# Performance work log

Hardware: AMD Instinct MI355X
Metric: run time of the kernel (lower is better)

Reference implementation:

```python
import jax, jax.numpy as jnp
import numpy as np
from jax import lax

EPSILON = 1e-12


def _sobel_kernels(n1=1, n2=2, n3=2):
    Sx = np.asarray([[[-n1, 0, n1], [-n2, 0, n2], [-n1, 0, n1]],
                     [[-n2, 0, n2], [-n3 * n2, 0, n3 * n2], [-n2, 0, n2]],
                     [[-n1, 0, n1], [-n2, 0, n2], [-n1, 0, n1]]])
    Sy = np.asarray([[[-n1, -n2, -n1], [0, 0, 0], [n1, n2, n1]],
                     [[-n2, -n3 * n2, -n2], [0, 0, 0], [n2, n3 * n2, n2]],
                     [[-n1, -n2, -n1], [0, 0, 0], [n1, n2, n1]]])
    Sz = np.asarray([[[-n1, -n2, -n1], [-n2, -n3 * n2, -n2], [-n1, -n2, -n1]],
                     [[0, 0, 0], [0, 0, 0], [0, 0, 0]],
                     [[n1, n2, n1], [n2, n3 * n2, n2], [n1, n2, n1]]])
    Sd11 = np.asarray([[[0, n1, n2], [-n1, 0, n1], [-n2, -n1, 0]],
                       [[0, n2, n2 * n3], [-n2, 0, n2], [-n2 * n3, -n2, 0]],
                       [[0, n1, n2], [-n1, 0, n1], [-n2, -n1, 0]]])
    Sd12 = np.asarray([[[-n2, -n1, 0], [-n1, 0, n1], [0, n1, n2]],
                       [[-n2 * n3, -n2, 0], [-n2, 0, n2], [0, n2, n2 * n3]],
                       [[-n2, -n1, 0], [-n1, 0, n1], [0, n1, n2]]])
    Sd21 = Sd11.T
    Sd22 = Sd12.T
    Sd31 = np.asarray([-S.T for S in Sd11.T])
    Sd32 = np.asarray([S.T for S in Sd12.T])
    ks = np.stack([Sx, Sy, Sz, Sd11, Sd12, Sd21, Sd22, Sd31, Sd32]).astype(np.float32)
    return jnp.asarray(ks[:, None])  # [9, 1, 3, 3, 3] (OIDHW)


_KERNELS = _sobel_kernels(1, 2, 2)


def _edge_magnitude(img):
    # img: [B, C, H, W, D]. Per-channel convs are summed over C in the original;
    # by linearity of conv, sum channels first, then run all 9 stencils at once.
    C = img.shape[1]
    x = jnp.sum(img, axis=1, keepdims=True)  # [B, 1, H, W, D]
    g = lax.conv_general_dilated(
        x, _KERNELS, window_strides=(1, 1, 1), padding='SAME',
        dimension_numbers=('NCDHW', 'OIDHW', 'NCDHW'))  # [B, 9, H, W, D]
    mag = jnp.sqrt(jnp.sum(g * g, axis=1, keepdims=True) + EPSILON)
    return mag / C  # (1/C) * sqrt(sum_sq + eps), matches operator precedence


def setup_inputs() -> dict:
    key = jax.random.key(0)
    k1, k2 = jax.random.split(key)
    shape = (2, 2, 128, 128, 128)
    y = jax.random.normal(k1, shape, dtype=jnp.float32)
    yp = jax.random.normal(k2, shape, dtype=jnp.float32)
    return {"y": y, "yp": yp}


def reference(y, yp):
    y_edge = _edge_magnitude(y)
    yp_edge = _edge_magnitude(yp)
    return jnp.mean((y_edge - yp_edge) ** 2)  # nn.MSELoss default 'mean'
```

## Files before the change

### kernel.cpp

```cpp
#include <hip/hip_runtime.h>


namespace {

constexpr int YX = 128 * 128;
constexpr ptrdiff_t CS = (ptrdiff_t)128 * YX;
constexpr int ZC = 16;
constexpr float INV_N = 1.0f / 4194304.0f;

__device__ __forceinline__ float edge_mag_half(const float* __restrict__ Ca,
                                               const float* __restrict__ Cb,
                                               const float* __restrict__ Cc) {
  const float g1  = __builtin_fmaf(2.0f, Cb[0], Ca[0] + Cc[0]);
  const float g2  = __builtin_fmaf(2.0f, Cb[1], Ca[1] + Cc[1]);
  const float g3  = Cc[2] - Ca[2];
  const float Azx = __builtin_fmaf(2.0f, Cb[3], Ca[3] + Cc[3]);
  const float Azy = __builtin_fmaf(2.0f, Cb[4], Ca[4] + Cc[4]);
  const float Axz = Cc[5] - Ca[5];
  const float Axy = g2 - Cb[1];
  const float Ayx = g1 - Cb[0];
  const float Ayz = Cc[6] - Ca[6];
  const float g4 = Azx - Azy, g5 = Azx + Azy;
  const float g6 = Axz - Axy, g7 = Axz + Axy;
  const float g8 = Ayx - Ayz, g9 = Ayx + Ayz;
  float s = __builtin_fmaf(g1, g1, 1e-12f);
  s = __builtin_fmaf(g2, g2, s); s = __builtin_fmaf(g3, g3, s);
  s = __builtin_fmaf(g4, g4, s); s = __builtin_fmaf(g5, g5, s);
  s = __builtin_fmaf(g6, g6, s); s = __builtin_fmaf(g7, g7, s);
  s = __builtin_fmaf(g8, g8, s); s = __builtin_fmaf(g9, g9, s);
  return 0.5f * sqrtf(s);
}

__device__ __forceinline__ void combos7(const float* __restrict__ s,
                                        const float* __restrict__ h,
                                        bool l0, bool l63, int seg,
                                        float* __restrict__ C) {
  const float t  = s[0] + s[2];
  const float ys = __builtin_fmaf(2.0f, s[1], t);
  const float ye = t + s[1];
  const float yd = s[2] - s[0];
  const float th  = h[0] + h[2];
  const float hys = __builtin_fmaf(2.0f, h[1], th);
  const float hye = th + h[1];
  const float hyd = h[2] - h[0];
  float ysL = __shfl_up(ys, 1),  ydL = __shfl_up(yd, 1),  yeL = __shfl_up(ye, 1);
  float ysR = __shfl_down(ys, 1), ydR = __shfl_down(yd, 1), yeR = __shfl_down(ye, 1);
  const float eLs = seg ? hys : 0.0f, eLd = seg ? hyd : 0.0f, eLe = seg ? hye : 0.0f;
  const float eRs = seg ? 0.0f : hys, eRd = seg ? 0.0f : hyd, eRe = seg ? 0.0f : hye;
  ysL = l0 ? eLs : ysL;  ydL = l0 ? eLd : ydL;  yeL = l0 ? eLe : yeL;
  ysR = l63 ? eRs : ysR; ydR = l63 ? eRd : ydR; yeR = l63 ? eRe : yeR;
  C[0] = ysR - ysL;
  const float tds = ydL + ydR;
  C[1] = __builtin_fmaf(2.0f, yd, tds);
  C[4] = tds + yd;
  const float tss = ysL + ysR;
  C[2] = __builtin_fmaf(2.0f, ys, tss);
  C[6] = tss + ys;
  C[3] = yeR - yeL;
  const float tes = yeL + yeR;
  C[5] = __builtin_fmaf(2.0f, ye, tes);
}

__global__ __launch_bounds__(256)
void gme_loss_kernel(const float* __restrict__ y,
                     const float* __restrict__ yp,
                     float* __restrict__ out) {
  const int tid  = threadIdx.x;
  const int lane = tid & 63;
  const int wv   = tid >> 6;
  const int yy   = blockIdx.x * 4 + wv;
  const int seg  = blockIdx.y >> 3;
  const int z0   = (blockIdx.y & 7) * ZC;
  const int b    = blockIdx.z;
  const int px   = seg * 64 + lane;
  const bool l0 = (lane == 0), l63 = (lane == 63);
  const bool isEdge = seg ? l0 : l63;
  const ptrdiff_t hd = seg ? -1 : 1;
  const float w0 = (yy > 0)   ? 1.0f : 0.0f;
  const float w2 = (yy < 127) ? 1.0f : 0.0f;
  const int r0 = (yy > 0) ? yy - 1 : 0;
  const int r2 = (yy < 127) ? yy + 1 : 127;

  const float* Yb = y  + (ptrdiff_t)b * 2 * CS;
  const float* Pb = yp + (ptrdiff_t)b * 2 * CS;
  const ptrdiff_t o0 = (ptrdiff_t)r0 * 128 + px;
  const ptrdiff_t o1 = (ptrdiff_t)yy * 128 + px;
  const ptrdiff_t o2 = (ptrdiff_t)r2 * 128 + px;

  float arA[12], arB[12], hr[12];
#pragma unroll
  for (int j = 0; j < 12; ++j) { arA[j] = 0.f; arB[j] = 0.f; hr[j] = 0.f; }

  auto issue_ar = [&](int zl, float* __restrict__ a) {
    if ((unsigned)zl < 128u) {
      const float* Yz = Yb + (ptrdiff_t)zl * YX;
      const float* Pz = Pb + (ptrdiff_t)zl * YX;
      a[0]  = Yz[o0]; a[1]  = Yz[o0 + CS];
      a[2]  = Yz[o1]; a[3]  = Yz[o1 + CS];
      a[4]  = Yz[o2]; a[5]  = Yz[o2 + CS];
      a[6]  = Pz[o0]; a[7]  = Pz[o0 + CS];
      a[8]  = Pz[o1]; a[9]  = Pz[o1 + CS];
      a[10] = Pz[o2]; a[11] = Pz[o2 + CS];
    } else {
#pragma unroll
      for (int j = 0; j < 12; ++j) a[j] = 0.0f;
    }
  };
  auto issue_hr = [&](int zl) {
    if ((unsigned)zl < 128u) {
      if (isEdge) {
        const float* Yz = Yb + (ptrdiff_t)zl * YX;
        const float* Pz = Pb + (ptrdiff_t)zl * YX;
        hr[0]  = Yz[o0 + hd]; hr[1]  = Yz[o0 + CS + hd];
        hr[2]  = Yz[o1 + hd]; hr[3]  = Yz[o1 + CS + hd];
        hr[4]  = Yz[o2 + hd]; hr[5]  = Yz[o2 + CS + hd];
        hr[6]  = Pz[o0 + hd]; hr[7]  = Pz[o0 + CS + hd];
        hr[8]  = Pz[o1 + hd]; hr[9]  = Pz[o1 + CS + hd];
        hr[10] = Pz[o2 + hd]; hr[11] = Pz[o2 + CS + hd];
      }
    } else {
#pragma unroll
      for (int j = 0; j < 12; ++j) hr[j] = 0.0f;
    }
  };

  float sY[3], hY[3], sP[3], hP[3];
  auto consume = [&](const float* __restrict__ a) {
    sY[0] = (a[0] + a[1])  * w0;  sY[1] = a[2] + a[3];  sY[2] = (a[4] + a[5])  * w2;
    sP[0] = (a[6] + a[7])  * w0;  sP[1] = a[8] + a[9];  sP[2] = (a[10] + a[11]) * w2;
    hY[0] = (hr[0] + hr[1]) * w0; hY[1] = hr[2] + hr[3]; hY[2] = (hr[4] + hr[5]) * w2;
    hP[0] = (hr[6] + hr[7]) * w0; hP[1] = hr[8] + hr[9]; hP[2] = (hr[10] + hr[11]) * w2;
  };

  float KY[3][7], KP[3][7];
  float acc = 0.0f;

  issue_ar(z0 - 1, arA);
  issue_hr(z0 - 1);
  issue_ar(z0, arB);

#pragma unroll 6
  for (int i = 0; i < ZC + 2; ++i) {
    const int zc = z0 - 1 + i;
    consume((i & 1) ? arB : arA);
    const int zl_hr = (i <= ZC)     ? (zc + 1) : 128;
    const int zl_ar = (i <= ZC - 1) ? (zc + 2) : 128;
    issue_hr(zl_hr);
    issue_ar(zl_ar, (i & 1) ? arB : arA);
    combos7(sY, hY, l0, l63, seg, KY[i % 3]);
    combos7(sP, hP, l0, l63, seg, KP[i % 3]);
    if (i >= 2) {
      const float my = edge_mag_half(KY[(i + 1) % 3], KY[(i + 2) % 3], KY[i % 3]);
      const float mp = edge_mag_half(KP[(i + 1) % 3], KP[(i + 2) % 3], KP[i % 3]);
      const float d = my - mp;
      acc = __builtin_fmaf(d, d, acc);
    }
  }

#pragma unroll
  for (int off = 32; off > 0; off >>= 1) acc += __shfl_down(acc, off);
  __shared__ float red[4];
  if (lane == 0) red[wv] = acc;
  __syncthreads();
  if (tid == 0) atomicAdd(out, (red[0] + red[1] + red[2] + red[3]) * INV_N);
}

}

extern "C" void kernel_launch(void* const* d_in, const int* in_sizes, int n_in,
                              void* d_out, int out_size, void* d_ws, size_t ws_size,
                              hipStream_t stream) {
  const float* y  = (const float*)d_in[0];
  const float* yp = (const float*)d_in[1];
  float* out = (float*)d_out;

  hipMemsetAsync(out, 0, sizeof(float), stream);

  dim3 block(256, 1, 1);
  dim3 grid(32,
            16,
            2);
  gme_loss_kernel<<<grid, block, 0, stream>>>(y, yp, out);
}
```

Baseline: 123.4 us.

## Process two x-columns per lane to drop halo loads and vectorize

Each lane now owns two adjacent x positions, so one wavefront covers a full 128-wide row. This removes the split into two x-segments and the extra edge-lane halo loads, and turns the loads into 8-byte float2 accesses. The z-chunk per block is halved to keep the same grid size, the z loop is fully unrolled, and launch bounds request 3 blocks per CU. Register pressure roughly doubles because every value is now a pair, which could cut occupancy. The shorter z chunk also raises the fraction of redundant z-halo reads per block.

After: 171.7 us. 39.2% more time.

```diff
diff --git a/kernel.cpp b/kernel.cpp
--- a/kernel.cpp
+++ b/kernel.cpp
@@ -5,63 +5,71 @@
 
 constexpr int YX = 128 * 128;
 constexpr ptrdiff_t CS = (ptrdiff_t)128 * YX;
-constexpr int ZC = 16;
+constexpr int ZC = 8;
 constexpr float INV_N = 1.0f / 4194304.0f;
 
-__device__ __forceinline__ float edge_mag_half(const float* __restrict__ Ca,
-                                               const float* __restrict__ Cb,
-                                               const float* __restrict__ Cc) {
-  const float g1  = __builtin_fmaf(2.0f, Cb[0], Ca[0] + Cc[0]);
-  const float g2  = __builtin_fmaf(2.0f, Cb[1], Ca[1] + Cc[1]);
-  const float g3  = Cc[2] - Ca[2];
-  const float Azx = __builtin_fmaf(2.0f, Cb[3], Ca[3] + Cc[3]);
-  const float Azy = __builtin_fmaf(2.0f, Cb[4], Ca[4] + Cc[4]);
-  const float Axz = Cc[5] - Ca[5];
-  const float Axy = g2 - Cb[1];
-  const float Ayx = g1 - Cb[0];
-  const float Ayz = Cc[6] - Ca[6];
-  const float g4 = Azx - Azy, g5 = Azx + Azy;
-  const float g6 = Axz - Axy, g7 = Axz + Axy;
-  const float g8 = Ayx - Ayz, g9 = Ayx + Ayz;
-  float s = __builtin_fmaf(g1, g1, 1e-12f);
-  s = __builtin_fmaf(g2, g2, s); s = __builtin_fmaf(g3, g3, s);
-  s = __builtin_fmaf(g4, g4, s); s = __builtin_fmaf(g5, g5, s);
-  s = __builtin_fmaf(g6, g6, s); s = __builtin_fmaf(g7, g7, s);
-  s = __builtin_fmaf(g8, g8, s); s = __builtin_fmaf(g9, g9, s);
-  return 0.5f * sqrtf(s);
+struct V2 { float x, y; };
+__device__ __forceinline__ V2 v2(float a, float b) { V2 r; r.x = a; r.y = b; return r; }
+__device__ __forceinline__ V2 operator+(V2 a, V2 b) { return v2(a.x + b.x, a.y + b.y); }
+__device__ __forceinline__ V2 operator-(V2 a, V2 b) { return v2(a.x - b.x, a.y - b.y); }
+__device__ __forceinline__ V2 operator*(float a, V2 b) { return v2(a * b.x, a * b.y); }
+__device__ __forceinline__ V2 fma2(float a, V2 b, V2 c) {
+  return v2(__builtin_fmaf(a, b.x, c.x), __builtin_fmaf(a, b.y, c.y));
+}
+__device__ __forceinline__ V2 fma2v(V2 a, V2 b, V2 c) {
+  return v2(__builtin_fmaf(a.x, b.x, c.x), __builtin_fmaf(a.y, b.y, c.y));
 }
 
-__device__ __forceinline__ void combos7(const float* __restrict__ s,
-                                        const float* __restrict__ h,
-                                        bool l0, bool l63, int seg,
-                                        float* __restrict__ C) {
-  const float t  = s[0] + s[2];
-  const float ys = __builtin_fmaf(2.0f, s[1], t);
-  const float ye = t + s[1];
-  const float yd = s[2] - s[0];
-  const float th  = h[0] + h[2];
-  const float hys = __builtin_fmaf(2.0f, h[1], th);
-  const float hye = th + h[1];
-  const float hyd = h[2] - h[0];
-  float ysL = __shfl_up(ys, 1),  ydL = __shfl_up(yd, 1),  yeL = __shfl_up(ye, 1);
-  float ysR = __shfl_down(ys, 1), ydR = __shfl_down(yd, 1), yeR = __shfl_down(ye, 1);
-  const float eLs = seg ? hys : 0.0f, eLd = seg ? hyd : 0.0f, eLe = seg ? hye : 0.0f;
-  const float eRs = seg ? 0.0f : hys, eRd = seg ? 0.0f : hyd, eRe = seg ? 0.0f : hye;
-  ysL = l0 ? eLs : ysL;  ydL = l0 ? eLd : ydL;  yeL = l0 ? eLe : yeL;
-  ysR = l63 ? eRs : ysR; ydR = l63 ? eRd : ydR; yeR = l63 ? eRe : yeR;
+__device__ __forceinline__ V2 edge_mag_half(const V2* __restrict__ Ca,
+                                            const V2* __restrict__ Cb,
+                                            const V2* __restrict__ Cc) {
+  const V2 g1  = fma2(2.0f, Cb[0], Ca[0] + Cc[0]);
+  const V2 g2  = fma2(2.0f, Cb[1], Ca[1] + Cc[1]);
+  const V2 g3  = Cc[2] - Ca[2];
+  const V2 Azx = fma2(2.0f, Cb[3], Ca[3] + Cc[3]);
+  const V2 Azy = fma2(2.0f, Cb[4], Ca[4] + Cc[4]);
+  const V2 Axz = Cc[5] - Ca[5];
+  const V2 Axy = g2 - Cb[1];
+  const V2 Ayx = g1 - Cb[0];
+  const V2 Ayz = Cc[6] - Ca[6];
+  const V2 g4 = Azx - Azy, g5 = Azx + Azy;
+  const V2 g6 = Axz - Axy, g7 = Axz + Axy;
+  const V2 g8 = Ayx - Ayz, g9 = Ayx + Ayz;
+  V2 s = fma2v(g1, g1, v2(1e-12f, 1e-12f));
+  s = fma2v(g2, g2, s); s = fma2v(g3, g3, s);
+  s = fma2v(g4, g4, s); s = fma2v(g5, g5, s);
+  s = fma2v(g6, g6, s); s = fma2v(g7, g7, s);
+  s = fma2v(g8, g8, s); s = fma2v(g9, g9, s);
+  return v2(0.5f * sqrtf(s.x), 0.5f * sqrtf(s.y));
+}
+
+__device__ __forceinline__ void combos7(V2 s0, V2 s1, V2 s2,
+                                        bool l0, bool l63,
+                                        V2* __restrict__ C) {
+  const V2 t  = s0 + s2;
+  const V2 ys = fma2(2.0f, s1, t);
+  const V2 ye = t + s1;
+  const V2 yd = s2 - s0;
+  float ysLx = __shfl_up(ys.y, 1),  ydLx = __shfl_up(yd.y, 1),  yeLx = __shfl_up(ye.y, 1);
+  float ysRy = __shfl_down(ys.x, 1), ydRy = __shfl_down(yd.x, 1), yeRy = __shfl_down(ye.x, 1);
+  if (l0)  { ysLx = 0.0f; ydLx = 0.0f; yeLx = 0.0f; }
+  if (l63) { ysRy = 0.0f; ydRy = 0.0f; yeRy = 0.0f; }
+  const V2 ysL = v2(ysLx, ys.x), ysR = v2(ys.y, ysRy);
+  const V2 ydL = v2(ydLx, yd.x), ydR = v2(yd.y, ydRy);
+  const V2 yeL = v2(yeLx, ye.x), yeR = v2(ye.y, yeRy);
   C[0] = ysR - ysL;
-  const float tds = ydL + ydR;
-  C[1] = __builtin_fmaf(2.0f, yd, tds);
+  const V2 tds = ydL + ydR;
+  C[1] = fma2(2.0f, yd, tds);
   C[4] = tds + yd;
-  const float tss = ysL + ysR;
-  C[2] = __builtin_fmaf(2.0f, ys, tss);
+  const V2 tss = ysL + ysR;
+  C[2] = fma2(2.0f, ys, tss);
   C[6] = tss + ys;
   C[3] = yeR - yeL;
-  const float tes = yeL + yeR;
-  C[5] = __builtin_fmaf(2.0f, ye, tes);
+  const V2 tes = yeL + yeR;
+  C[5] = fma2(2.0f, ye, tes);
 }
 
-__global__ __launch_bounds__(256)
+__global__ __launch_bounds__(256, 3)
 void gme_loss_kernel(const float* __restrict__ y,
                      const float* __restrict__ yp,
                      float* __restrict__ out) {
@@ -69,13 +77,10 @@
   const int lane = tid & 63;
   const int wv   = tid >> 6;
   const int yy   = blockIdx.x * 4 + wv;
-  const int seg  = blockIdx.y >> 3;
-  const int z0   = (blockIdx.y & 7) * ZC;
+  const int z0   = blockIdx.y * ZC;
   const int b    = blockIdx.z;
-  const int px   = seg * 64 + lane;
+  const int px   = 2 * lane;
   const bool l0 = (lane == 0), l63 = (lane == 63);
-  const bool isEdge = seg ? l0 : l63;
-  const ptrdiff_t hd = seg ? -1 : 1;
   const float w0 = (yy > 0)   ? 1.0f : 0.0f;
   const float w2 = (yy < 127) ? 1.0f : 0.0f;
   const int r0 = (yy > 0) ? yy - 1 : 0;
@@ -83,77 +88,55 @@
 
   const float* Yb = y  + (ptrdiff_t)b * 2 * CS;
   const float* Pb = yp + (ptrdiff_t)b * 2 * CS;
-  const ptrdiff_t o0 = (ptrdiff_t)r0 * 128 + px;
-  const ptrdiff_t o1 = (ptrdiff_t)yy * 128 + px;
-  const ptrdiff_t o2 = (ptrdiff_t)r2 * 128 + px;
+  const int o0 = r0 * 128 + px;
+  const int o1 = yy * 128 + px;
+  const int o2 = r2 * 128 + px;
 
-  float arA[12], arB[12], hr[12];
+  V2 arA[12], arB[12];
 #pragma unroll
-  for (int j = 0; j < 12; ++j) { arA[j] = 0.f; arB[j] = 0.f; hr[j] = 0.f; }
+  for (int j = 0; j < 12; ++j) { arA[j] = v2(0.f, 0.f); arB[j] = v2(0.f, 0.f); }
 
-  auto issue_ar = [&](int zl, float* __restrict__ a) {
+  auto issue = [&](int zl, V2* __restrict__ a) {
     if ((unsigned)zl < 128u) {
       const float* Yz = Yb + (ptrdiff_t)zl * YX;
       const float* Pz = Pb + (ptrdiff_t)zl * YX;
-      a[0]  = Yz[o0]; a[1]  = Yz[o0 + CS];
-      a[2]  = Yz[o1]; a[3]  = Yz[o1 + CS];
-      a[4]  = Yz[o2]; a[5]  = Yz[o2 + CS];
-      a[6]  = Pz[o0]; a[7]  = Pz[o0 + CS];
-      a[8]  = Pz[o1]; a[9]  = Pz[o1 + CS];
-      a[10] = Pz[o2]; a[11] = Pz[o2 + CS];
+      a[0]  = *(const V2*)(Yz + o0); a[1]  = *(const V2*)(Yz + o0 + CS);
+      a[2]  = *(const V2*)(Yz + o1); a[3]  = *(const V2*)(Yz + o1 + CS);
+      a[4]  = *(const V2*)(Yz + o2); a[5]  = *(const V2*)(Yz + o2 + CS);
+      a[6]  = *(const V2*)(Pz + o0); a[7]  = *(const V2*)(Pz + o0 + CS);
+      a[8]  = *(const V2*)(Pz + o1); a[9]  = *(const V2*)(Pz + o1 + CS);
+      a[10] = *(const V2*)(Pz + o2); a[11] = *(const V2*)(Pz + o2 + CS);
     } else {
 #pragma unroll
-      for (int j = 0; j < 12; ++j) a[j] = 0.0f;
-    }
-  };
-  auto issue_hr = [&](int zl) {
-    if ((unsigned)zl < 128u) {
-      if (isEdge) {
-        const float* Yz = Yb + (ptrdiff_t)zl * YX;
-        const float* Pz = Pb + (ptrdiff_t)zl * YX;
-        hr[0]  = Yz[o0 + hd]; hr[1]  = Yz[o0 + CS + hd];
-        hr[2]  = Yz[o1 + hd]; hr[3]  = Yz[o1 + CS + hd];
-        hr[4]  = Yz[o2 + hd]; hr[5]  = Yz[o2 + CS + hd];
-        hr[6]  = Pz[o0 + hd]; hr[7]  = Pz[o0 + CS + hd];
-        hr[8]  = Pz[o1 + hd]; hr[9]  = Pz[o1 + CS + hd];
-        hr[10] = Pz[o2 + hd]; hr[11] = Pz[o2 + CS + hd];
-      }
-    } else {
-#pragma unroll
-      for (int j = 0; j < 12; ++j) hr[j] = 0.0f;
+      for (int j = 0; j < 12; ++j) a[j] = v2(0.f, 0.f);
     }
   };
 
-  float sY[3], hY[3], sP[3], hP[3];
-  auto consume = [&](const float* __restrict__ a) {
-    sY[0] = (a[0] + a[1])  * w0;  sY[1] = a[2] + a[3];  sY[2] = (a[4] + a[5])  * w2;
-    sP[0] = (a[6] + a[7])  * w0;  sP[1] = a[8] + a[9];  sP[2] = (a[10] + a[11]) * w2;
-    hY[0] = (hr[0] + hr[1]) * w0; hY[1] = hr[2] + hr[3]; hY[2] = (hr[4] + hr[5]) * w2;
-    hP[0] = (hr[6] + hr[7]) * w0; hP[1] = hr[8] + hr[9]; hP[2] = (hr[10] + hr[11]) * w2;
-  };
-
-  float KY[3][7], KP[3][7];
+  V2 KY[3][7], KP[3][7];
   float acc = 0.0f;
 
-  issue_ar(z0 - 1, arA);
-  issue_hr(z0 - 1);
-  issue_ar(z0, arB);
+  issue(z0 - 1, arA);
+  issue(z0,     arB);
 
-#pragma unroll 6
+#pragma unroll
   for (int i = 0; i < ZC + 2; ++i) {
     const int zc = z0 - 1 + i;
-    consume((i & 1) ? arB : arA);
-    const int zl_hr = (i <= ZC)     ? (zc + 1) : 128;
-    const int zl_ar = (i <= ZC - 1) ? (zc + 2) : 128;
-    issue_hr(zl_hr);
-    issue_ar(zl_ar, (i & 1) ? arB : arA);
-    combos7(sY, hY, l0, l63, seg, KY[i % 3]);
-    combos7(sP, hP, l0, l63, seg, KP[i % 3]);
+    V2* a = (i & 1) ? arB : arA;
+    const V2 sY0 = w0 * (a[0] + a[1]);
+    const V2 sY1 = a[2] + a[3];
+    const V2 sY2 = w2 * (a[4] + a[5]);
+    const V2 sP0 = w0 * (a[6] + a[7]);
+    const V2 sP1 = a[8] + a[9];
+    const V2 sP2 = w2 * (a[10] + a[11]);
+    issue((i <= ZC - 1) ? (zc + 2) : 128, a);
+    combos7(sY0, sY1, sY2, l0, l63, KY[i % 3]);
+    combos7(sP0, sP1, sP2, l0, l63, KP[i % 3]);
     if (i >= 2) {
-      const float my = edge_mag_half(KY[(i + 1) % 3], KY[(i + 2) % 3], KY[i % 3]);
-      const float mp = edge_mag_half(KP[(i + 1) % 3], KP[(i + 2) % 3], KP[i % 3]);
-      const float d = my - mp;
-      acc = __builtin_fmaf(d, d, acc);
+      const V2 my = edge_mag_half(KY[(i + 1) % 3], KY[(i + 2) % 3], KY[i % 3]);
+      const V2 mp = edge_mag_half(KP[(i + 1) % 3], KP[(i + 2) % 3], KP[i % 3]);
+      const V2 d = my - mp;
+      acc = __builtin_fmaf(d.x, d.x, acc);
+      acc = __builtin_fmaf(d.y, d.y, acc);
     }
   }
 
```
